# Optimization experiments

Hardware: AMD Instinct MI355X
Metric: run time of the kernel (lower is better)

Reference implementation:

```python
import jax, jax.numpy as jnp
from jax import lax
import numpy as np

B, T, N = 128, 4096, 32
SMOOTH = 1.0


def setup_inputs() -> dict:
    key = jax.random.key(0)
    k1, k2, k3, k4 = jax.random.split(key, 4)
    potentials = jax.random.normal(k1, (B, T, N), dtype=jnp.float32)
    y_true = jax.random.randint(k2, (B, T), 0, N)
    lengths = jax.random.randint(k3, (B,), 1, T + 1)
    transitions = jax.random.normal(k4, (N, N), dtype=jnp.float32) * 0.1
    return {"potentials": potentials, "y_true": y_true,
            "lengths": lengths, "transitions": transitions}


def crf_marginals(potentials, lengths, transitions):
    """Linear-chain CRF posterior marginals p(y_t = k | x), shape [B, T, N]."""
    Bq, Tq, Nq = potentials.shape
    lengths = lengths.astype(jnp.int32)
    # valid[t-1, b] == (t < lengths[b]) for t = 1..T-1
    valid = jnp.arange(1, Tq)[:, None] < lengths[None, :]  # [T-1, B]
    pots_t = jnp.transpose(potentials[:, 1:], (1, 0, 2))    # [T-1, B, N]

    # forward recursion (carry alpha unchanged past sequence end)
    def fwd_step(alpha_prev, inp):
        pot_t, v = inp
        new = jax.nn.logsumexp(alpha_prev[:, :, None] + transitions[None], axis=1) + pot_t
        alpha = jnp.where(v[:, None], new, alpha_prev)
        return alpha, alpha

    alpha0 = potentials[:, 0]
    _, alphas_rest = lax.scan(fwd_step, alpha0, (pots_t, valid))
    alphas = jnp.concatenate([alpha0[None], alphas_rest], axis=0)  # [T, B, N]

    # backward recursion (beta = 0 at/after the last valid position)
    def bwd_step(beta_next, inp):
        pot_next, v = inp  # pot_next is potentials at t+1; v == (t+1 < length)
        new = jax.nn.logsumexp(transitions[None] + (pot_next + beta_next)[:, None, :], axis=2)
        beta = jnp.where(v[:, None], new, jnp.zeros_like(new))
        return beta, beta

    beta_last = jnp.zeros((Bq, Nq), dtype=potentials.dtype)
    _, betas_rest = lax.scan(bwd_step, beta_last, (pots_t, valid), reverse=True)
    betas = jnp.concatenate([betas_rest, beta_last[None]], axis=0)  # [T, B, N]

    # since alpha is frozen past the end, alphas[-1] == alpha_{length-1}
    logZ = jax.nn.logsumexp(alphas[-1], axis=-1)  # [B]
    log_marg = alphas + betas - logZ[None, :, None]
    return jnp.exp(jnp.transpose(log_marg, (1, 0, 2)))  # [B, T, N]


def reference(potentials, y_true, lengths, transitions):
    probs = crf_marginals(potentials, lengths, transitions)
    num_tags = probs.shape[-1]
    y_oh = jax.nn.one_hot(y_true.astype(jnp.int32), num_tags, dtype=probs.dtype)
    Tq = probs.shape[1]
    mask_btn = (jnp.arange(Tq)[None, :] < lengths.astype(jnp.int32)[:, None]
                ).astype(probs.dtype)[:, :, None]
    y_m = y_oh * mask_btn
    p_m = probs * mask_btn
    inter = jnp.sum(y_m * p_m, axis=(1, 2))
    sums = jnp.sum(y_m, axis=(1, 2)) + jnp.sum(p_m, axis=(1, 2))
    dice = (2.0 * inter + SMOOTH) / (sums + SMOOTH)
    return 1.0 - dice
```

## Files before the change

kernel.cpp:

```cpp
#include <hip/hip_runtime.h>
#include <hip/hip_bf16.h>

#define Bq 128
#define Tq 4096
#define Nq 32
#define SEGL 128
#define NSEG 32
#define BURN 16
#define TRIPB 15
#define UNR 4
#define NBLK 36
#define LOG2E 1.4426950408889634f

typedef float v2f __attribute__((ext_vector_type(2)));
typedef unsigned short u16;

__device__ __forceinline__ unsigned pack_bf16(float f0, float f1) {
  unsigned u0 = __float_as_uint(f0);
  unsigned u1 = __float_as_uint(f1);
  u0 = u0 + 0x7fffu + ((u0 >> 16) & 1u);
  u1 = u1 + 0x7fffu + ((u1 >> 16) & 1u);
  return (u0 >> 16) | (u1 & 0xffff0000u);
}

extern "C" __global__ void __launch_bounds__(256)
crf_chain_kernel(const float* __restrict__ pot, const int* __restrict__ lengths,
                 const float* __restrict__ trans,
                 u16* __restrict__ eaF, u16* __restrict__ eaB,
                 float* __restrict__ iacc) {
  __shared__ unsigned xbuf[16][16];
  const int tid = threadIdx.x;
  if (blockIdx.x == 0 && tid < Bq) iacc[tid] = 0.f;

  const int cslot = tid >> 4;
  const int sub = tid & 15;
  const int oc = sub * 2;
  const int cid = blockIdx.x * 16 + cslot;
  const int b = cid >> 6;
  const int dir = (cid >> 5) & 1;
  const int s = cid & 31;
  const int len = lengths[b];
  const int sL = s * SEGL;
  const bool active = (sL < len);
  if (__ballot(active) == 0ull) return;

  const int lenm1 = len - 1;
  const int tend = min(sL + SEGL, len);
  const int end = tend - 1;
  const int t1 = min(lenm1, end + BURN);
  const int dstep = dir ? -1 : 1;
  const int cst = dir ? (end + BURN) : ((s == 0) ? (1 - TRIPB) : (sL - BURN + 1));
  const int skip = dir ? (end + BURN - t1) : ((s == 0) ? TRIPB : 0);
  const int wlo = sL;
  const int whi = dir ? min(end, t1) : end;
  const unsigned uspan = (unsigned)(whi - wlo);

  v2f eTa[16], eTb[16];
#pragma unroll
  for (int k = 0; k < 16; ++k) {
    const int i0 = 2 * k, i1 = 2 * k + 1;
    float a0 = dir ? trans[oc * Nq + i0] : trans[i0 * Nq + oc];
    float a1 = dir ? trans[oc * Nq + i1] : trans[i1 * Nq + oc];
    float b0 = dir ? trans[(oc + 1) * Nq + i0] : trans[i0 * Nq + oc + 1];
    float b1 = dir ? trans[(oc + 1) * Nq + i1] : trans[i1 * Nq + oc + 1];
    v2f ea, eb;
    ea.x = exp2f(a0 * LOG2E); ea.y = exp2f(a1 * LOG2E);
    eb.x = exp2f(b0 * LOG2E); eb.y = exp2f(b1 * LOG2E);
    eTa[k] = ea; eTb[k] = eb;
  }

  const float* pb = pot + (size_t)b * Tq * Nq;
  float raw0, raw1;
  if (dir) { raw0 = 1.f; raw1 = 1.f; }
  else {
    const int rinit = (s == 0) ? 0 : (sL - BURN);
    raw0 = exp2f(pb[rinit * Nq + oc] * LOG2E);
    raw1 = exp2f(pb[rinit * Nq + oc + 1] * LOG2E);
  }
  u16* outbase = (dir ? eaB : eaF) + ((size_t)b * Tq) * Nq + oc;
  if (!dir) { if (active && s == 0) *(unsigned*)outbase = pack_bf16(raw0, raw1); }
  else      { if (active && t1 <= end) *(unsigned*)(outbase + (size_t)t1 * Nq) = pack_bf16(1.f, 1.f); }

  int cb = cst;
  int r = cst - dir;
  u16* outp = outbase + (ptrdiff_t)r * Nq;
  v2f pn[UNR];
#pragma unroll
  for (int k = 0; k < UNR; ++k) {
    int cc = min(max(cb + dstep * k, 0), lenm1);
    pn[k] = *(const v2f*)(pb + cc * Nq + oc);
  }

  int g0 = 0;
#pragma unroll 1
  for (int blk = 0; blk < NBLK; ++blk) {
    v2f pc[UNR];
#pragma unroll
    for (int k = 0; k < UNR; ++k) pc[k] = pn[k];
#pragma unroll
    for (int k = 0; k < UNR; ++k) {
      int cc = min(max(cb + dstep * (k + UNR), 0), lenm1);
      pn[k] = *(const v2f*)(pb + cc * Nq + oc);
    }
#pragma unroll
    for (int k = 0; k < UNR; ++k) {
      float ep0 = exp2f(pc[k].x * LOG2E);
      float ep1 = exp2f(pc[k].y * LOG2E);
      float w0 = dir ? raw0 * ep0 : raw0;
      float w1 = dir ? raw1 * ep1 : raw1;
      xbuf[cslot][sub] = pack_bf16(w0, w1);
      const uint4* xb4 = (const uint4*)&xbuf[cslot][0];
      uint4 B0 = xb4[0], B1 = xb4[1], B2 = xb4[2], B3 = xb4[3];
      int eb = (int)((B0.x << 16) & 0x7f800000u);
      float corr = __int_as_float(0x7f000000 - eb);
      v2f a0, a1, a2, a3, d0, d1, d2, d3;
      a0 = 0.f; a1 = 0.f; a2 = 0.f; a3 = 0.f;
      d0 = 0.f; d1 = 0.f; d2 = 0.f; d3 = 0.f;
#define ACC(dw, p, A, D) { v2f xp; \
      xp.x = __uint_as_float((dw) << 16); \
      xp.y = __uint_as_float((dw) & 0xffff0000u); \
      A += xp * eTa[p]; D += xp * eTb[p]; }
      ACC(B0.x, 0, a0, d0) ACC(B0.y, 1, a1, d1) ACC(B0.z, 2, a2, d2) ACC(B0.w, 3, a3, d3)
      ACC(B1.x, 4, a0, d0) ACC(B1.y, 5, a1, d1) ACC(B1.z, 6, a2, d2) ACC(B1.w, 7, a3, d3)
      ACC(B2.x, 8, a0, d0) ACC(B2.y, 9, a1, d1) ACC(B2.z,10, a2, d2) ACC(B2.w,11, a3, d3)
      ACC(B3.x,12, a0, d0) ACC(B3.y,13, a1, d1) ACC(B3.z,14, a2, d2) ACC(B3.w,15, a3, d3)
#undef ACC
      v2f sa = (a0 + a1) + (a2 + a3);
      v2f sd = (d0 + d1) + (d2 + d3);
      float s0 = sa.x + sa.y;
      float s1 = sd.x + sd.y;
      float n0 = s0 * corr * (dir ? 1.f : ep0);
      float n1 = s1 * corr * (dir ? 1.f : ep1);
      const bool upd = (g0 + k) >= skip;
      raw0 = upd ? n0 : raw0;
      raw1 = upd ? n1 : raw1;
      if (active && (unsigned)(r - wlo) <= uspan) *(unsigned*)outp = pack_bf16(raw0, raw1);
      outp += dstep * Nq;
      r += dstep;
    }
    cb += dstep * UNR;
    g0 += UNR;
  }
}

extern "C" __global__ void __launch_bounds__(256)
dice_kernel(const u16* __restrict__ eaF, const u16* __restrict__ eaB,
            const int* __restrict__ y, const int* __restrict__ lengths,
            float* __restrict__ iacc) {
  const int b = blockIdx.x >> 4;
  const int q = blockIdx.x & 15;
  const int len = lengths[b];
  if (q * 256 >= len) return;
  const int t = q * 256 + threadIdx.x;
  float I = 0.f;
  if (t < len) {
    const size_t base = ((size_t)b * Tq + t) * Nq;
    const uint4* a4 = (const uint4*)(eaF + base);
    const uint4* b4 = (const uint4*)(eaB + base);
    float c0 = 0.f, c1 = 0.f, c2 = 0.f, c3 = 0.f;
#pragma unroll
    for (int w = 0; w < 4; ++w) {
      uint4 ua = a4[w], ub = b4[w];
      c0 = fmaf(__uint_as_float(ua.x << 16), __uint_as_float(ub.x << 16), c0);
      c1 = fmaf(__uint_as_float(ua.x & 0xffff0000u), __uint_as_float(ub.x & 0xffff0000u), c1);
      c2 = fmaf(__uint_as_float(ua.y << 16), __uint_as_float(ub.y << 16), c2);
      c3 = fmaf(__uint_as_float(ua.y & 0xffff0000u), __uint_as_float(ub.y & 0xffff0000u), c3);
      c0 = fmaf(__uint_as_float(ua.z << 16), __uint_as_float(ub.z << 16), c0);
      c1 = fmaf(__uint_as_float(ua.z & 0xffff0000u), __uint_as_float(ub.z & 0xffff0000u), c1);
      c2 = fmaf(__uint_as_float(ua.w << 16), __uint_as_float(ub.w << 16), c2);
      c3 = fmaf(__uint_as_float(ua.w & 0xffff0000u), __uint_as_float(ub.w & 0xffff0000u), c3);
    }
    float v = (c0 + c1) + (c2 + c3);
    int yt = y[(size_t)b * Tq + t];
    float ay = __uint_as_float(((unsigned)eaF[base + yt]) << 16);
    float by = __uint_as_float(((unsigned)eaB[base + yt]) << 16);
    I = (ay * by) / v;
  }
#pragma unroll
  for (int m = 1; m < 64; m <<= 1) I += __shfl_xor(I, m);
  __shared__ float sI[4];
  if ((threadIdx.x & 63) == 0) sI[threadIdx.x >> 6] = I;
  __syncthreads();
  if (threadIdx.x == 0) atomicAdd(&iacc[b], sI[0] + sI[1] + sI[2] + sI[3]);
}

extern "C" __global__ void final_kernel(const float* __restrict__ iacc,
                                        const int* __restrict__ lengths,
                                        float* __restrict__ out) {
  const int b = threadIdx.x;
  if (b < Bq) out[b] = 1.f - (2.f * iacc[b] + 1.f) / (2.f * (float)lengths[b] + 1.f);
}

extern "C" void kernel_launch(void* const* d_in, const int* in_sizes, int n_in,
                              void* d_out, int out_size, void* d_ws, size_t ws_size,
                              hipStream_t stream) {
  const float* pot = (const float*)d_in[0];
  const int* y_true = (const int*)d_in[1];
  const int* lengths = (const int*)d_in[2];
  const float* trans = (const float*)d_in[3];
  float* out = (float*)d_out;

  char* ws = (char*)d_ws;
  const size_t n_elems = (size_t)Bq * Tq * Nq;
  u16* eaF = (u16*)ws;
  u16* eaB = (u16*)(ws + n_elems * 2);
  float* iacc = (float*)(ws + n_elems * 4);

  crf_chain_kernel<<<512, 256, 0, stream>>>(pot, lengths, trans, eaF, eaB, iacc);
  dice_kernel<<<Bq * 16, 256, 0, stream>>>(eaF, eaB, y_true, lengths, iacc);
  final_kernel<<<1, 128, 0, stream>>>(iacc, lengths, out);
}
```

Measured before the change: 185.7 us.

## Halve CRF chain segments, shrink blocks to one wave, use hardware bf16 pack

Splits each sequence into 64 segments of 64 steps instead of 32 of 128, which halves the serial recurrence length per chain and launches one-wavefront blocks with 4 chains each. Rescaling by the leading exponent is moved out of the inner step to once per 4-step block. The software bf16 rounding is replaced with the v_cvt_pk_bf16_f32 instruction, and the accumulator tree is cut from four partial sums to two. The trade-off is more total burn-in work and more chains, plus a possible range risk from less frequent renormalisation.

```diff
diff --git a/kernel.cpp b/kernel.cpp
--- a/kernel.cpp
+++ b/kernel.cpp
@@ -4,52 +4,49 @@
 #define Bq 128
 #define Tq 4096
 #define Nq 32
-#define SEGL 128
-#define NSEG 32
+#define SEGL 64
+#define NSEG 64
 #define BURN 16
 #define TRIPB 15
 #define UNR 4
-#define NBLK 36
+#define NBLK 20
 #define LOG2E 1.4426950408889634f
 
 typedef float v2f __attribute__((ext_vector_type(2)));
 typedef unsigned short u16;
 
-__device__ __forceinline__ unsigned pack_bf16(float f0, float f1) {
-  unsigned u0 = __float_as_uint(f0);
-  unsigned u1 = __float_as_uint(f1);
-  u0 = u0 + 0x7fffu + ((u0 >> 16) & 1u);
-  u1 = u1 + 0x7fffu + ((u1 >> 16) & 1u);
-  return (u0 >> 16) | (u1 & 0xffff0000u);
-}
-
-extern "C" __global__ void __launch_bounds__(256)
+__device__ __forceinline__ unsigned cvt_pk_bf16(float lo, float hi) {
+  unsigned r;
+  asm("v_cvt_pk_bf16_f32 %0, %1, %2" : "=v"(r) : "v"(lo), "v"(hi));
+  return r;
+}
+
+extern "C" __global__ void __launch_bounds__(64, 4)
 crf_chain_kernel(const float* __restrict__ pot, const int* __restrict__ lengths,
                  const float* __restrict__ trans,
                  u16* __restrict__ eaF, u16* __restrict__ eaB,
                  float* __restrict__ iacc) {
-  __shared__ unsigned xbuf[16][16];
+  __shared__ unsigned xbuf[4][16];
   const int tid = threadIdx.x;
-  if (blockIdx.x == 0 && tid < Bq) iacc[tid] = 0.f;
+  if (blockIdx.x < 2) iacc[blockIdx.x * 64 + tid] = 0.f;
 
   const int cslot = tid >> 4;
   const int sub = tid & 15;
-  const int oc = sub * 2;
-  const int cid = blockIdx.x * 16 + cslot;
-  const int b = cid >> 6;
-  const int dir = (cid >> 5) & 1;
-  const int s = cid & 31;
+  const int oc = sub << 1;
+  const int cid = (blockIdx.x << 2) + cslot;
+  const int b = cid >> 7;
+  const int dir = (cid >> 6) & 1;
+  const int s = cid & 63;
   const int len = lengths[b];
   const int sL = s * SEGL;
   const bool active = (sL < len);
-  if (__ballot(active) == 0ull) return;
+  if (!__ballot(active)) return;
 
   const int lenm1 = len - 1;
-  const int tend = min(sL + SEGL, len);
-  const int end = tend - 1;
+  const int end = min(sL + SEGL, len) - 1;
   const int t1 = min(lenm1, end + BURN);
   const int dstep = dir ? -1 : 1;
-  const int cst = dir ? (end + BURN) : ((s == 0) ? (1 - TRIPB) : (sL - BURN + 1));
+  const int cst = dir ? (end + BURN) : ((s == 0) ? (1 - TRIPB) : (sL - TRIPB));
   const int skip = dir ? (end + BURN - t1) : ((s == 0) ? TRIPB : 0);
   const int wlo = sL;
   const int whi = dir ? min(end, t1) : end;
@@ -61,12 +58,10 @@
     const int i0 = 2 * k, i1 = 2 * k + 1;
     float a0 = dir ? trans[oc * Nq + i0] : trans[i0 * Nq + oc];
     float a1 = dir ? trans[oc * Nq + i1] : trans[i1 * Nq + oc];
-    float b0 = dir ? trans[(oc + 1) * Nq + i0] : trans[i0 * Nq + oc + 1];
-    float b1 = dir ? trans[(oc + 1) * Nq + i1] : trans[i1 * Nq + oc + 1];
-    v2f ea, eb;
-    ea.x = exp2f(a0 * LOG2E); ea.y = exp2f(a1 * LOG2E);
-    eb.x = exp2f(b0 * LOG2E); eb.y = exp2f(b1 * LOG2E);
-    eTa[k] = ea; eTb[k] = eb;
+    float c0 = dir ? trans[(oc + 1) * Nq + i0] : trans[i0 * Nq + oc + 1];
+    float c1 = dir ? trans[(oc + 1) * Nq + i1] : trans[i1 * Nq + oc + 1];
+    eTa[k].x = exp2f(a0 * LOG2E); eTa[k].y = exp2f(a1 * LOG2E);
+    eTb[k].x = exp2f(c0 * LOG2E); eTb[k].y = exp2f(c1 * LOG2E);
   }
 
   const float* pb = pot + (size_t)b * Tq * Nq;
@@ -77,23 +72,25 @@
     raw0 = exp2f(pb[rinit * Nq + oc] * LOG2E);
     raw1 = exp2f(pb[rinit * Nq + oc + 1] * LOG2E);
   }
-  u16* outbase = (dir ? eaB : eaF) + ((size_t)b * Tq) * Nq + oc;
-  if (!dir) { if (active && s == 0) *(unsigned*)outbase = pack_bf16(raw0, raw1); }
-  else      { if (active && t1 <= end) *(unsigned*)(outbase + (size_t)t1 * Nq) = pack_bf16(1.f, 1.f); }
-
+  int r = cst - dir;
   int cb = cst;
-  int r = cst - dir;
-  u16* outp = outbase + (ptrdiff_t)r * Nq;
+  u16* outp = (dir ? eaB : eaF) + (size_t)b * Tq * Nq + oc + (ptrdiff_t)r * Nq;
+  unsigned lb0 = 0x3f80u;
+
   v2f pn[UNR];
 #pragma unroll
   for (int k = 0; k < UNR; ++k) {
-    int cc = min(max(cb + dstep * k, 0), lenm1);
+    int cc = min(max(cst + dstep * k, 0), lenm1);
     pn[k] = *(const v2f*)(pb + cc * Nq + oc);
   }
 
-  int g0 = 0;
 #pragma unroll 1
   for (int blk = 0; blk < NBLK; ++blk) {
+    {
+      int ebits = (int)((lb0 << 16) & 0x7f800000u);
+      float corr = __int_as_float(0x7f000000 - ebits);
+      raw0 *= corr; raw1 *= corr;
+    }
     v2f pc[UNR];
 #pragma unroll
     for (int k = 0; k < UNR; ++k) pc[k] = pn[k];
@@ -102,44 +99,40 @@
       int cc = min(max(cb + dstep * (k + UNR), 0), lenm1);
       pn[k] = *(const v2f*)(pb + cc * Nq + oc);
     }
+    const int g0 = blk * UNR;
 #pragma unroll
     for (int k = 0; k < UNR; ++k) {
       float ep0 = exp2f(pc[k].x * LOG2E);
       float ep1 = exp2f(pc[k].y * LOG2E);
       float w0 = dir ? raw0 * ep0 : raw0;
       float w1 = dir ? raw1 * ep1 : raw1;
-      xbuf[cslot][sub] = pack_bf16(w0, w1);
-      const uint4* xb4 = (const uint4*)&xbuf[cslot][0];
+      xbuf[cslot][sub] = cvt_pk_bf16(w0, w1);
+      const uint4* xb4 = (const uint4*)(&xbuf[cslot][0]);
       uint4 B0 = xb4[0], B1 = xb4[1], B2 = xb4[2], B3 = xb4[3];
-      int eb = (int)((B0.x << 16) & 0x7f800000u);
-      float corr = __int_as_float(0x7f000000 - eb);
-      v2f a0, a1, a2, a3, d0, d1, d2, d3;
-      a0 = 0.f; a1 = 0.f; a2 = 0.f; a3 = 0.f;
-      d0 = 0.f; d1 = 0.f; d2 = 0.f; d3 = 0.f;
+      lb0 = B0.x;
+      v2f a0 = 0.f, a1 = 0.f, d0 = 0.f, d1 = 0.f;
 #define ACC(dw, p, A, D) { v2f xp; \
       xp.x = __uint_as_float((dw) << 16); \
       xp.y = __uint_as_float((dw) & 0xffff0000u); \
       A += xp * eTa[p]; D += xp * eTb[p]; }
-      ACC(B0.x, 0, a0, d0) ACC(B0.y, 1, a1, d1) ACC(B0.z, 2, a2, d2) ACC(B0.w, 3, a3, d3)
-      ACC(B1.x, 4, a0, d0) ACC(B1.y, 5, a1, d1) ACC(B1.z, 6, a2, d2) ACC(B1.w, 7, a3, d3)
-      ACC(B2.x, 8, a0, d0) ACC(B2.y, 9, a1, d1) ACC(B2.z,10, a2, d2) ACC(B2.w,11, a3, d3)
-      ACC(B3.x,12, a0, d0) ACC(B3.y,13, a1, d1) ACC(B3.z,14, a2, d2) ACC(B3.w,15, a3, d3)
+      ACC(B0.x, 0, a0, d0) ACC(B0.y, 1, a1, d1) ACC(B0.z, 2, a0, d0) ACC(B0.w, 3, a1, d1)
+      ACC(B1.x, 4, a0, d0) ACC(B1.y, 5, a1, d1) ACC(B1.z, 6, a0, d0) ACC(B1.w, 7, a1, d1)
+      ACC(B2.x, 8, a0, d0) ACC(B2.y, 9, a1, d1) ACC(B2.z,10, a0, d0) ACC(B2.w,11, a1, d1)
+      ACC(B3.x,12, a0, d0) ACC(B3.y,13, a1, d1) ACC(B3.z,14, a0, d0) ACC(B3.w,15, a1, d1)
 #undef ACC
-      v2f sa = (a0 + a1) + (a2 + a3);
-      v2f sd = (d0 + d1) + (d2 + d3);
-      float s0 = sa.x + sa.y;
-      float s1 = sd.x + sd.y;
-      float n0 = s0 * corr * (dir ? 1.f : ep0);
-      float n1 = s1 * corr * (dir ? 1.f : ep1);
+      v2f sa = a0 + a1, sd = d0 + d1;
+      float s0 = sa.x + sa.y, s1 = sd.x + sd.y;
+      float n0 = dir ? s0 : s0 * ep0;
+      float n1 = dir ? s1 : s1 * ep1;
       const bool upd = (g0 + k) >= skip;
       raw0 = upd ? n0 : raw0;
       raw1 = upd ? n1 : raw1;
-      if (active && (unsigned)(r - wlo) <= uspan) *(unsigned*)outp = pack_bf16(raw0, raw1);
+      if (active && (unsigned)(r - wlo) <= uspan)
+        *(unsigned*)outp = cvt_pk_bf16(raw0, raw1);
       outp += dstep * Nq;
       r += dstep;
     }
     cb += dstep * UNR;
-    g0 += UNR;
   }
 }
 
@@ -206,7 +199,7 @@
   u16* eaB = (u16*)(ws + n_elems * 2);
   float* iacc = (float*)(ws + n_elems * 4);
 
-  crf_chain_kernel<<<512, 256, 0, stream>>>(pot, lengths, trans, eaF, eaB, iacc);
+  crf_chain_kernel<<<Bq * 2 * NSEG / 4, 64, 0, stream>>>(pot, lengths, trans, eaF, eaB, iacc);
   dice_kernel<<<Bq * 16, 256, 0, stream>>>(eaF, eaB, y_true, lengths, iacc);
   final_kernel<<<1, 128, 0, stream>>>(iacc, lengths, out);
 }
```

Result: slower. 208.8 us (+12.5%).
